# Optimization experiments

Hardware: AMD Instinct MI355X
Metric: run time of the kernel (lower is better)

## Reference

```python
import jax, jax.numpy as jnp
import numpy as np

# ---- fixed architecture constants (from init_kwargs) ----
N_WALL, N_ROOF, N_WINDOW = 4, 1, 2
N_RC = N_WALL + N_ROOF
HID = 32
ENC_LEN = 48
DT = 900.0
R_OPAQUE, C_OPAQUE = 10.0, 1.0e5
R_TRANS = 2.0
DIRECT_COEF, ABS_WALL_COEF, ABS_ROOF_COEF = 0.5, 0.5, 0.5
C_ZONE = 1.0e5
B, T = 2048, 1440


def setup_inputs() -> dict:
    key = jax.random.key(0)
    k0, k1, k2 = jax.random.split(key, 3)
    input_X = jax.random.normal(k0, (B, T, 7), dtype=jnp.float32)
    # EnvelopeRC deterministic inits
    rc_R_inv = jnp.concatenate([
        1.0 / (10.0 + 1.0 * jnp.arange(N_WALL, dtype=jnp.float32)),
        1.0 / (20.0 + 2.0 * jnp.arange(N_ROOF, dtype=jnp.float32))])
    rc_C_inv = jnp.concatenate([
        1.0 / (80.0 + 10.0 * jnp.arange(N_WALL, dtype=jnp.float32)),
        1.0 / (60.0 + 10.0 * jnp.arange(N_ROOF, dtype=jnp.float32))])
    window_R_inv = 1.0 / (1.0 + 0.1 * jnp.arange(N_WINDOW, dtype=jnp.float32))
    # Internal MLP: xavier_uniform with gain 0.1, zero bias
    lim1 = 0.1 * np.sqrt(6.0 / (2 + HID))
    int_W1 = jax.random.uniform(k1, (HID, 2), jnp.float32, -lim1, lim1)
    int_b1 = jnp.zeros((HID,), jnp.float32)
    lim2 = 0.1 * np.sqrt(6.0 / (HID + 1))
    int_W2 = jax.random.uniform(k2, (1, HID), jnp.float32, -lim2, lim2)
    int_b2 = jnp.zeros((1,), jnp.float32)
    return {
        'input_X': input_X,
        'rc_R_inv': rc_R_inv, 'rc_C_inv': rc_C_inv, 'window_R_inv': window_R_inv,
        'hvac_gain': jnp.float32(0.1),
        'int_W1': int_W1, 'int_b1': int_b1, 'int_W2': int_W2, 'int_b2': int_b2,
        'int_gain': jnp.float32(0.1),
        'direct_gain': jnp.float32(0.1), 'abs_wall': jnp.float32(0.1), 'abs_roof': jnp.float32(0.1),
        'zone_C_inv': jnp.float32(1.0 / 10000.0),
    }


def _forward(input_X, rc_R_inv, rc_C_inv, window_R_inv, hvac_gain,
             int_W1, int_b1, int_W2, int_b2, int_gain,
             direct_gain, abs_wall, abs_roof, zone_C_inv):
    sp = jax.nn.softplus
    Bn, Tn = input_X.shape[0], input_X.shape[1]
    tz_gt  = input_X[:, :, 0]   # [B,T]
    t_amb  = input_X[:, :, 1]
    sol    = input_X[:, :, 2]
    int_x  = input_X[:, :, 3:6]
    hvac_x = input_X[:, :, 6]

    # Internal MLP (state-free -> vectorized over time)
    h1  = jax.nn.relu(jnp.einsum('bti,hi->bth', int_x[:, :, :2], int_W1) + int_b1)
    sch = jax.nn.sigmoid(jnp.einsum('bth,oh->bto', h1, int_W2) + int_b2)[:, :, 0] + int_x[:, :, 2]
    q_int  = sp(int_gain) * 0.1 * sch          # [B,T]
    q_hvac = sp(hvac_gain) * 0.1 * hvac_x      # [B,T]

    # Bounded RC parameters
    r_inv   = sp(rc_R_inv) * (1.0 / R_OPAQUE)  # [n_rc]
    c_inv   = sp(rc_C_inv) * (1.0 / C_OPAQUE)  # [n_rc]
    win_rsum = jnp.sum(sp(window_R_inv)) * (1.0 / R_TRANS)
    abs_rc  = jnp.where(jnp.arange(N_RC) < N_WALL,
                        sp(abs_wall) * ABS_WALL_COEF,
                        sp(abs_roof) * ABS_ROOF_COEF)   # [n_rc]
    q_dir   = sp(direct_gain) * DIRECT_COEF * sol       # [B,T]
    cz_inv  = sp(zone_C_inv) * (1.0 / C_ZONE)

    # Initial state: Tmid_i = 0.7*Tzone0 + 0.3*Tamb0
    Tz0   = tz_gt[:, 0]                                      # [B]
    Tmid0 = jnp.broadcast_to((0.7 * Tz0 + 0.3 * t_amb[:, 0])[:, None], (Bn, N_RC))

    # Teacher forcing during encoder window: carry GT zone temp while t+1 < enc_len
    tz_gt_next = jnp.concatenate([tz_gt[:, 1:], tz_gt[:, -1:]], axis=1)  # [B,T]
    use_gt = (jnp.arange(Tn) + 1) < ENC_LEN                              # [T]

    xs = (t_amb.T, sol.T, q_dir.T, q_int.T, q_hvac.T, tz_gt_next.T, use_gt)

    def step(carry, x):
        Tz, Tmid = carry                      # [B], [B,n_rc]
        ta, so, qd, qi, qh, gt_next, ug = x
        q_in  = (ta[:, None] - Tmid) * r_inv
        q_out = (Tmid - Tz[:, None]) * r_inv
        dTmid = (q_in - q_out + so[:, None] * abs_rc) * c_inv
        q_env = jnp.sum(q_out, axis=1) + (ta - Tz) * win_rsum
        dTz   = (q_env + qi + qh + qd) * cz_inv
        Tz_new   = Tz + dTz * DT
        Tmid_new = Tmid + dTmid * DT
        Tz_carry = jnp.where(ug, gt_next, Tz_new)
        return (Tz_carry, Tmid_new), Tz_new

    _, tz_seq = jax.lax.scan(step, (Tz0, Tmid0), xs)   # [T,B]
    return jnp.transpose(tz_seq)[:, :, None]           # [B,T,1]


def reference(input_X, rc_R_inv, rc_C_inv, window_R_inv, hvac_gain,
              int_W1, int_b1, int_W2, int_b2, int_gain,
              direct_gain, abs_wall, abs_roof, zone_C_inv):
    return _forward(input_X, rc_R_inv, rc_C_inv, window_R_inv, hvac_gain,
                    int_W1, int_b1, int_W2, int_b2, int_gain,
                    direct_gain, abs_wall, abs_roof, zone_C_inv)
```

## Files before the change

kernel.cpp:

```cpp
#include <hip/hip_runtime.h>
#include <math.h>

#define BATCH 2048
#define TLEN  1440
#define T7    (TLEN * 7)
#define CL0   48
#define CL2   16
#define NCH   88
#define TREST (TLEN - CL0)

#define PACK2_OFF 0
#define PACKU_OFF (PACK2_OFF + 2 * TLEN * BATCH)
#define PACKG_OFF (PACKU_OFF + TLEN * BATCH)
#define INIT_OFF  (PACKG_OFF + 48 * BATCH)
#define E_OFF     (INIT_OFF + 2 * BATCH)
#define XC_OFF    (E_OFF + NCH * BATCH * 8)
#define A16_OFF   (XC_OFF + NCH * BATCH * 8)
#define V_OFF     (A16_OFF + 64)
#define WP_OFF    (V_OFF + 128)
#define PRM_OFF   (WP_OFF + 128)
#define WS_FLOATS (PRM_OFF + 32)

__device__ __forceinline__ float sp_precise(float x) { return log1pf(expf(x)); }

struct Prm {
  float P[5], M[5], Q[5], K[5];
  float AZ, dtczw, dtcz, cInt, cHv, cDir;
};
__device__ __forceinline__ Prm make_prm(const float* rcR, const float* rcC,
                                        const float* winR, const float* hvg,
                                        const float* ing, const float* dg,
                                        const float* aw, const float* ar,
                                        const float* zc) {
  Prm p;
  float r[5], cc[5], rsum = 0.f;
  #pragma unroll
  for (int j = 0; j < 5; ++j) {
    r[j] = sp_precise(rcR[j]) * 0.1f;
    cc[j] = sp_precise(rcC[j]) * 1e-5f;
    rsum += r[j];
  }
  float w  = (sp_precise(winR[0]) + sp_precise(winR[1])) * 0.5f;
  float cz = sp_precise(zc[0]) * 1e-5f;
  float aW = sp_precise(aw[0]) * 0.5f, aR = sp_precise(ar[0]) * 0.5f;
  float dtcz = 900.f * cz;
  #pragma unroll
  for (int j = 0; j < 5; ++j) {
    p.P[j] = 900.f * r[j] * cc[j];
    p.M[j] = 1.f - 2.f * p.P[j];
    p.Q[j] = 900.f * cc[j] * ((j < 4) ? aW : aR);
    p.K[j] = dtcz * r[j];
  }
  p.AZ = 1.f - dtcz * (w + rsum);
  p.dtczw = dtcz * w;
  p.dtcz = dtcz;
  p.cInt = sp_precise(ing[0]) * 0.1f;
  p.cHv  = sp_precise(hvg[0]) * 0.1f;
  p.cDir = sp_precise(dg[0])  * 0.5f;
  return p;
}

__global__ void k0_params(const float* __restrict__ rcR, const float* __restrict__ rcC,
                          const float* __restrict__ winR, const float* __restrict__ hvg,
                          const float* __restrict__ W1, const float* __restrict__ B1,
                          const float* __restrict__ W2, const float* __restrict__ B2,
                          const float* __restrict__ ing, const float* __restrict__ dg,
                          const float* __restrict__ aw, const float* __restrict__ ar,
                          const float* __restrict__ zc, float* __restrict__ ws) {
  __shared__ float A0s[36], Ma[36], Mb[36], vrow[2][8];
  int ln = threadIdx.x;
  if (ln < 32) {
    ((float4*)(ws + WP_OFF))[ln] =
        make_float4(W1[2 * ln], W1[2 * ln + 1], B1[ln], W2[ln]);
  }
  if (ln == 0) {
    Prm p = make_prm(rcR, rcC, winR, hvg, ing, dg, aw, ar, zc);
    float* prm = ws + PRM_OFF;
    for (int j = 0; j < 5; ++j) {
      prm[j] = p.P[j]; prm[5 + j] = p.M[j]; prm[10 + j] = p.Q[j]; prm[15 + j] = p.K[j];
    }
    prm[20] = p.AZ; prm[21] = p.dtczw; prm[22] = p.dtcz;
    prm[23] = p.cInt; prm[24] = p.cHv; prm[25] = p.cDir;
    prm[26] = B2[0];
    for (int i = 0; i < 36; ++i) A0s[i] = 0.f;
    A0s[0] = p.AZ;
    for (int j = 0; j < 5; ++j) {
      A0s[0 * 6 + 1 + j]       = p.K[j];
      A0s[(1 + j) * 6 + 0]     = p.P[j];
      A0s[(1 + j) * 6 + 1 + j] = p.M[j];
    }
  }
  __syncthreads();
  int i6 = ln / 6, j6 = ln % 6;
  bool act = ln < 36;
#define MM(DST, L, R) { if (act) { float s = 0.f; \
  for (int m = 0; m < 6; ++m) s = fmaf((L)[i6 * 6 + m], (R)[m * 6 + j6], s); \
  (DST)[ln] = s; } __syncthreads(); }
  MM(Mb, A0s, A0s);
  MM(Ma, Mb, Mb);
  MM(Mb, Ma, Ma);
  MM(Ma, Mb, Mb);
  if (act) ws[A16_OFF + ln] = Ma[ln];
  if (ln < 6) vrow[0][ln] = A0s[ln];
  __syncthreads();
  int cur = 0;
  for (int kk = 0; kk < CL2; ++kk) {
    if (ln < 6) {
      ws[V_OFF + kk * 8 + ln] = vrow[cur][ln];
      float s = 0.f;
      for (int m = 0; m < 6; ++m) s = fmaf(vrow[cur][m], A0s[m * 6 + ln], s);
      vrow[1 - cur][ln] = s;
    }
    __syncthreads();
    cur ^= 1;
  }
}

__global__ __launch_bounds__(256) void k1_pack(const float* __restrict__ X,
                                               float* __restrict__ ws) {
  __shared__ float lds[256 * 29];
  __shared__ float ldsW[128];
  int tg  = blockIdx.x >> 3;
  int b0  = (blockIdx.x & 7) << 8;
  int t0r = tg * 4;
  int tid = threadIdx.x;
  int b   = b0 + tid;
  const float* prm = ws + PRM_OFF;
  float dtczw = prm[21], dtcz = prm[22];
  float cInt = prm[23], cHv = prm[24], cDir = prm[25];
  float b2 = prm[26];
  if (tid < 32) *(float4*)&ldsW[tid * 4] = ((const float4*)(ws + WP_OFF))[tid];
  const float* base = X + ((size_t)b0 * TLEN + t0r) * 7;
  #pragma unroll
  for (int i = 0; i < 7; ++i) {
    int F = i * 256 + tid;
    int row = F / 7, q = F - row * 7;
    float4 v = *(const float4*)(base + (size_t)row * T7 + q * 4);
    int la = row * 29 + q * 4;
    lds[la] = v.x; lds[la + 1] = v.y; lds[la + 2] = v.z; lds[la + 3] = v.w;
  }
  float gtb = 0.f;
  if (t0r < 44) gtb = X[(size_t)b * T7 + (size_t)(t0r + 4) * 7];
  __syncthreads();
  int j29 = tid * 29;
  float ta[4], so[4], x3[4], x4[4], x5[4], hv[4];
  #pragma unroll
  for (int s = 0; s < 4; ++s) {
    const float* x = &lds[j29 + s * 7];
    ta[s] = x[1]; so[s] = x[2]; x3[s] = x[3]; x4[s] = x[4]; x5[s] = x[5]; hv[s] = x[6];
  }
  float acc[4] = {b2, b2, b2, b2};
  #pragma unroll
  for (int h = 0; h < 32; ++h) {
    float4 wv = *(const float4*)&ldsW[h * 4];
    #pragma unroll
    for (int s = 0; s < 4; ++s) {
      float z = fmaf(wv.x, x3[s], fmaf(wv.y, x4[s], wv.z));
      acc[s] = fmaf(wv.w, fmaxf(z, 0.f), acc[s]);
    }
  }
  float2* pk2 = (float2*)(ws + PACK2_OFF);
  float*  pu  = ws + PACKU_OFF;
  float*  pg  = ws + PACKG_OFF;
  #pragma unroll
  for (int s = 0; s < 4; ++s) {
    float sch = __frcp_rn(1.f + __expf(-acc[s])) + x5[s];
    float q = fmaf(cInt, sch, fmaf(cHv, hv[s], cDir * so[s]));
    float u = fmaf(dtczw, ta[s], dtcz * q);
    int t = t0r + s;
    size_t o = (size_t)t * BATCH + b;
    pk2[o] = make_float2(ta[s], so[s]);
    pu[o]  = u;
    if (t < 48) {
      float gt = (t < 47) ? ((s < 3) ? lds[j29 + (s + 1) * 7] : gtb) : 0.f;
      pg[o] = gt;
    }
  }
  if (tg == 0) {
    float tz0 = lds[j29], ta0 = lds[j29 + 1];
    ((float2*)(ws + INIT_OFF))[b] = make_float2(tz0, fmaf(0.7f, tz0, 0.3f * ta0));
  }
}

__global__ __launch_bounds__(256) void k2_scan(float* __restrict__ out,
                                               float* __restrict__ ws) {
  int c = blockIdx.x >> 3;
  int b = ((blockIdx.x & 7) << 8) + threadIdx.x;
  const float* prm = ws + PRM_OFF;
  float Pa[5], Mm[5], Qa[5], Ka[5];
  #pragma unroll
  for (int j = 0; j < 5; ++j) {
    Pa[j] = prm[j]; Mm[j] = prm[5 + j]; Qa[j] = prm[10 + j]; Ka[j] = prm[15 + j];
  }
  float AZ = prm[20];
  bool isc0 = (c == 0);
  int t0 = isc0 ? 0 : CL0 + (c - 1) * CL2;
  int steps = isc0 ? CL0 : CL2;
  float Tz = 0.f, T0 = 0.f, T1 = 0.f, T2 = 0.f, T3 = 0.f, T4 = 0.f;
  if (isc0) {
    float2 iv = ((const float2*)(ws + INIT_OFF))[b];
    Tz = iv.x;
    T0 = T1 = T2 = T3 = T4 = iv.y;
  }
  const float2* pk2 = ((const float2*)(ws + PACK2_OFF)) + (size_t)t0 * BATCH + b;
  const float*  pu  = ws + PACKU_OFF + (size_t)t0 * BATCH + b;
  const float*  pg  = ws + PACKG_OFF + b;
  float* op = out + (size_t)b * TLEN + t0;
  float o0 = 0.f, o1 = 0.f, o2 = 0.f;
  #pragma unroll 4
  for (int k = 0; k < steps; ++k) {
    float2 f2 = pk2[(size_t)k * BATCH];
    float  uv = pu[(size_t)k * BATCH];
    float d = fmaf(Ka[0], T0, uv);
    d = fmaf(Ka[1], T1, d); d = fmaf(Ka[2], T2, d);
    d = fmaf(Ka[3], T3, d); d = fmaf(Ka[4], T4, d);
    float tzn = fmaf(AZ, Tz, d);
    T0 = fmaf(Mm[0], T0, fmaf(Pa[0], Tz, fmaf(Pa[0], f2.x, Qa[0] * f2.y)));
    T1 = fmaf(Mm[1], T1, fmaf(Pa[1], Tz, fmaf(Pa[1], f2.x, Qa[1] * f2.y)));
    T2 = fmaf(Mm[2], T2, fmaf(Pa[2], Tz, fmaf(Pa[2], f2.x, Qa[2] * f2.y)));
    T3 = fmaf(Mm[3], T3, fmaf(Pa[3], Tz, fmaf(Pa[3], f2.x, Qa[3] * f2.y)));
    T4 = fmaf(Mm[4], T4, fmaf(Pa[4], Tz, fmaf(Pa[4], f2.x, Qa[4] * f2.y)));
    int ph = k & 3;
    if (ph == 0) o0 = tzn; else if (ph == 1) o1 = tzn;
    else if (ph == 2) o2 = tzn;
    else *(float4*)(op + (k - 3)) = make_float4(o0, o1, o2, tzn);
    if (isc0 && k < 47) Tz = pg[(size_t)k * BATCH];
    else Tz = tzn;
  }
  float* e = ws + E_OFF + ((size_t)c * BATCH + b) * 8;
  *(float4*)e       = make_float4(Tz, T0, T1, T2);
  *(float4*)(e + 4) = make_float4(T3, T4, 0.f, 0.f);
}

__global__ __launch_bounds__(64) void k2b_combine(float* __restrict__ ws) {
  int b = blockIdx.x * 64 + threadIdx.x;
  float A16r[36];
  #pragma unroll
  for (int i = 0; i < 36; ++i) A16r[i] = ws[A16_OFF + i];
  const float* e = ws + E_OFF;
  float4 h0 = *(const float4*)(e + (size_t)b * 8);
  float2 h1 = *(const float2*)(e + (size_t)b * 8 + 4);
  float Xs[6] = {h0.x, h0.y, h0.z, h0.w, h1.x, h1.y};
  for (int base = 1; base <= 87; base += 8) {
    float4 q0[8]; float2 q1[8];
    #pragma unroll
    for (int i = 0; i < 8; ++i) {
      int cI = base + i;
      if (cI <= 86) {
        const float* en = e + ((size_t)cI * BATCH + b) * 8;
        q0[i] = *(const float4*)en;
        q1[i] = *(const float2*)(en + 4);
      }
    }
    #pragma unroll
    for (int i = 0; i < 8; ++i) {
      int cI = base + i;
      if (cI > 87) break;
      float* xc = ws + XC_OFF + ((size_t)cI * BATCH + b) * 8;
      *(float4*)xc       = make_float4(Xs[0], Xs[1], Xs[2], Xs[3]);
      *(float2*)(xc + 4) = make_float2(Xs[4], Xs[5]);
      if (cI <= 86) {
        float ecur[6] = {q0[i].x, q0[i].y, q0[i].z, q0[i].w, q1[i].x, q1[i].y};
        float Y[6];
        #pragma unroll
        for (int r = 0; r < 6; ++r) {
          float s = ecur[r];
          #pragma unroll
          for (int m = 0; m < 6; ++m) s = fmaf(A16r[r * 6 + m], Xs[m], s);
          Y[r] = s;
        }
        #pragma unroll
        for (int j = 0; j < 6; ++j) Xs[j] = Y[j];
      }
    }
  }
}

__global__ __launch_bounds__(256) void k2c_correct(float* __restrict__ out,
                                                   const float* __restrict__ ws) {
  int tid = blockIdx.x * 256 + threadIdx.x;
  int b  = tid / TREST;
  int tt = tid - b * TREST;
  int c  = (tt >> 4) + 1;
  int kk = tt & 15;
  const float* xc = ws + XC_OFF + ((size_t)c * BATCH + b) * 8;
  float4 x0 = *(const float4*)xc;
  float2 x1 = *(const float2*)(xc + 4);
  const float* v = ws + V_OFF + kk * 8;
  float4 v0 = *(const float4*)v;
  float2 v1 = *(const float2*)(v + 4);
  size_t o = (size_t)b * TLEN + CL0 + tt;
  float s = out[o];
  s = fmaf(v0.x, x0.x, s); s = fmaf(v0.y, x0.y, s); s = fmaf(v0.z, x0.z, s);
  s = fmaf(v0.w, x0.w, s); s = fmaf(v1.x, x1.x, s); s = fmaf(v1.y, x1.y, s);
  out[o] = s;
}

__global__ void k_fallback(const float* __restrict__ X,
    const float* __restrict__ rcR, const float* __restrict__ rcC,
    const float* __restrict__ winR, const float* __restrict__ hvg,
    const float* __restrict__ W1, const float* __restrict__ B1,
    const float* __restrict__ W2, const float* __restrict__ B2,
    const float* __restrict__ ing, const float* __restrict__ dg,
    const float* __restrict__ aw, const float* __restrict__ ar,
    const float* __restrict__ zc, float* __restrict__ out) {
  int b = blockIdx.x * 64 + threadIdx.x;
  if (b >= BATCH) return;
  Prm p = make_prm(rcR, rcC, winR, hvg, ing, dg, aw, ar, zc);
  const float* xb = X + (size_t)b * T7;
  float Tz = xb[0];
  float tm = fmaf(0.7f, xb[0], 0.3f * xb[1]);
  float Tm[5] = {tm, tm, tm, tm, tm};
  for (int t = 0; t < TLEN; ++t) {
    const float* x = xb + t * 7;
    float ta = x[1], so = x[2], x3 = x[3], x4 = x[4], x5 = x[5], hv = x[6];
    float acc = B2[0];
    #pragma unroll
    for (int h = 0; h < 32; ++h) {
      float z = fmaf(W1[2 * h], x3, fmaf(W1[2 * h + 1], x4, B1[h]));
      acc = fmaf(W2[h], fmaxf(z, 0.f), acc);
    }
    float sch = __frcp_rn(1.f + __expf(-acc)) + x5;
    float q = fmaf(p.cInt, sch, fmaf(p.cHv, hv, p.cDir * so));
    float u = fmaf(p.dtczw, ta, p.dtcz * q);
    float d = u;
    #pragma unroll
    for (int j = 0; j < 5; ++j) d = fmaf(p.K[j], Tm[j], d);
    float tzn = fmaf(p.AZ, Tz, d);
    #pragma unroll
    for (int j = 0; j < 5; ++j)
      Tm[j] = fmaf(p.M[j], Tm[j], fmaf(p.P[j], Tz, fmaf(p.P[j], ta, p.Q[j] * so)));
    out[(size_t)b * TLEN + t] = tzn;
    Tz = (t < 47) ? x[7] : tzn;
  }
}

extern "C" void kernel_launch(void* const* d_in, const int* in_sizes, int n_in,
                              void* d_out, int out_size, void* d_ws, size_t ws_size,
                              hipStream_t stream) {
  const float* X    = (const float*)d_in[0];
  const float* rcR  = (const float*)d_in[1];
  const float* rcC  = (const float*)d_in[2];
  const float* winR = (const float*)d_in[3];
  const float* hvg  = (const float*)d_in[4];
  const float* W1   = (const float*)d_in[5];
  const float* B1   = (const float*)d_in[6];
  const float* W2   = (const float*)d_in[7];
  const float* B2   = (const float*)d_in[8];
  const float* ing  = (const float*)d_in[9];
  const float* dg   = (const float*)d_in[10];
  const float* aw   = (const float*)d_in[11];
  const float* ar   = (const float*)d_in[12];
  const float* zc   = (const float*)d_in[13];
  float* out = (float*)d_out;
  float* ws  = (float*)d_ws;

  if (ws_size >= (size_t)WS_FLOATS * sizeof(float)) {
    k0_params<<<1, 64, 0, stream>>>(rcR, rcC, winR, hvg, W1, B1, W2, B2,
                                    ing, dg, aw, ar, zc, ws);
    k1_pack<<<(TLEN / 4) * 8, 256, 0, stream>>>(X, ws);
    k2_scan<<<NCH * 8, 256, 0, stream>>>(out, ws);
    k2b_combine<<<32, 64, 0, stream>>>(ws);
    k2c_correct<<<(BATCH * TREST) / 256, 256, 0, stream>>>(out, ws);
  } else {
    k_fallback<<<BATCH / 64, 64, 0, stream>>>(X, rcR, rcC, winR, hvg, W1, B1, W2, B2,
                                              ing, dg, aw, ar, zc, out);
  }
}
```

Measured before the change: 214.9 us.

## Remove params kernel; recompute parameters per kernel and prefetch scan inputs

Drops the single-block parameter kernel and recomputes the softplus-derived coefficients inside each remaining kernel. The combine kernel now builds A^16 in registers, and the correction kernel computes its row vector by iterating up to 15 steps per thread. The scan kernel is split into a first-chunk branch and a generic branch, and each preloads 16 timesteps of packed inputs into registers before the recurrence. This removes one launch and a serial dependency but adds redundant transcendental and matrix math per thread, which is notable in the elementwise correction kernel.

```diff
diff --git a/kernel.cpp b/kernel.cpp
--- a/kernel.cpp
+++ b/kernel.cpp
@@ -15,11 +15,7 @@
 #define INIT_OFF  (PACKG_OFF + 48 * BATCH)
 #define E_OFF     (INIT_OFF + 2 * BATCH)
 #define XC_OFF    (E_OFF + NCH * BATCH * 8)
-#define A16_OFF   (XC_OFF + NCH * BATCH * 8)
-#define V_OFF     (A16_OFF + 64)
-#define WP_OFF    (V_OFF + 128)
-#define PRM_OFF   (WP_OFF + 128)
-#define WS_FLOATS (PRM_OFF + 32)
+#define WS_FLOATS (XC_OFF + NCH * BATCH * 8)
 
 __device__ __forceinline__ float sp_precise(float x) { return log1pf(expf(x)); }
 
@@ -60,64 +56,14 @@
   return p;
 }
 
-__global__ void k0_params(const float* __restrict__ rcR, const float* __restrict__ rcC,
-                          const float* __restrict__ winR, const float* __restrict__ hvg,
-                          const float* __restrict__ W1, const float* __restrict__ B1,
-                          const float* __restrict__ W2, const float* __restrict__ B2,
-                          const float* __restrict__ ing, const float* __restrict__ dg,
-                          const float* __restrict__ aw, const float* __restrict__ ar,
-                          const float* __restrict__ zc, float* __restrict__ ws) {
-  __shared__ float A0s[36], Ma[36], Mb[36], vrow[2][8];
-  int ln = threadIdx.x;
-  if (ln < 32) {
-    ((float4*)(ws + WP_OFF))[ln] =
-        make_float4(W1[2 * ln], W1[2 * ln + 1], B1[ln], W2[ln]);
-  }
-  if (ln == 0) {
-    Prm p = make_prm(rcR, rcC, winR, hvg, ing, dg, aw, ar, zc);
-    float* prm = ws + PRM_OFF;
-    for (int j = 0; j < 5; ++j) {
-      prm[j] = p.P[j]; prm[5 + j] = p.M[j]; prm[10 + j] = p.Q[j]; prm[15 + j] = p.K[j];
-    }
-    prm[20] = p.AZ; prm[21] = p.dtczw; prm[22] = p.dtcz;
-    prm[23] = p.cInt; prm[24] = p.cHv; prm[25] = p.cDir;
-    prm[26] = B2[0];
-    for (int i = 0; i < 36; ++i) A0s[i] = 0.f;
-    A0s[0] = p.AZ;
-    for (int j = 0; j < 5; ++j) {
-      A0s[0 * 6 + 1 + j]       = p.K[j];
-      A0s[(1 + j) * 6 + 0]     = p.P[j];
-      A0s[(1 + j) * 6 + 1 + j] = p.M[j];
-    }
-  }
-  __syncthreads();
-  int i6 = ln / 6, j6 = ln % 6;
-  bool act = ln < 36;
-#define MM(DST, L, R) { if (act) { float s = 0.f; \
-  for (int m = 0; m < 6; ++m) s = fmaf((L)[i6 * 6 + m], (R)[m * 6 + j6], s); \
-  (DST)[ln] = s; } __syncthreads(); }
-  MM(Mb, A0s, A0s);
-  MM(Ma, Mb, Mb);
-  MM(Mb, Ma, Ma);
-  MM(Ma, Mb, Mb);
-  if (act) ws[A16_OFF + ln] = Ma[ln];
-  if (ln < 6) vrow[0][ln] = A0s[ln];
-  __syncthreads();
-  int cur = 0;
-  for (int kk = 0; kk < CL2; ++kk) {
-    if (ln < 6) {
-      ws[V_OFF + kk * 8 + ln] = vrow[cur][ln];
-      float s = 0.f;
-      for (int m = 0; m < 6; ++m) s = fmaf(vrow[cur][m], A0s[m * 6 + ln], s);
-      vrow[1 - cur][ln] = s;
-    }
-    __syncthreads();
-    cur ^= 1;
-  }
-}
-
 __global__ __launch_bounds__(256) void k1_pack(const float* __restrict__ X,
-                                               float* __restrict__ ws) {
+    const float* __restrict__ rcR, const float* __restrict__ rcC,
+    const float* __restrict__ winR, const float* __restrict__ hvg,
+    const float* __restrict__ W1, const float* __restrict__ B1,
+    const float* __restrict__ W2, const float* __restrict__ B2,
+    const float* __restrict__ ing, const float* __restrict__ dg,
+    const float* __restrict__ aw, const float* __restrict__ ar,
+    const float* __restrict__ zc, float* __restrict__ ws) {
   __shared__ float lds[256 * 29];
   __shared__ float ldsW[128];
   int tg  = blockIdx.x >> 3;
@@ -125,11 +71,14 @@
   int t0r = tg * 4;
   int tid = threadIdx.x;
   int b   = b0 + tid;
-  const float* prm = ws + PRM_OFF;
-  float dtczw = prm[21], dtcz = prm[22];
-  float cInt = prm[23], cHv = prm[24], cDir = prm[25];
-  float b2 = prm[26];
-  if (tid < 32) *(float4*)&ldsW[tid * 4] = ((const float4*)(ws + WP_OFF))[tid];
+  Prm p = make_prm(rcR, rcC, winR, hvg, ing, dg, aw, ar, zc);
+  float b2 = B2[0];
+  if (tid < 32) {
+    ldsW[tid * 4 + 0] = W1[2 * tid];
+    ldsW[tid * 4 + 1] = W1[2 * tid + 1];
+    ldsW[tid * 4 + 2] = B1[tid];
+    ldsW[tid * 4 + 3] = W2[tid];
+  }
   const float* base = X + ((size_t)b0 * TLEN + t0r) * 7;
   #pragma unroll
   for (int i = 0; i < 7; ++i) {
@@ -165,8 +114,8 @@
   #pragma unroll
   for (int s = 0; s < 4; ++s) {
     float sch = __frcp_rn(1.f + __expf(-acc[s])) + x5[s];
-    float q = fmaf(cInt, sch, fmaf(cHv, hv[s], cDir * so[s]));
-    float u = fmaf(dtczw, ta[s], dtcz * q);
+    float q = fmaf(p.cInt, sch, fmaf(p.cHv, hv[s], p.cDir * so[s]));
+    float u = fmaf(p.dtczw, ta[s], p.dtcz * q);
     int t = t0r + s;
     size_t o = (size_t)t * BATCH + b;
     pk2[o] = make_float2(ta[s], so[s]);
@@ -182,61 +131,119 @@
   }
 }
 
-__global__ __launch_bounds__(256) void k2_scan(float* __restrict__ out,
-                                               float* __restrict__ ws) {
+__global__ __launch_bounds__(256) void k2_scan(
+    const float* __restrict__ rcR, const float* __restrict__ rcC,
+    const float* __restrict__ winR, const float* __restrict__ hvg,
+    const float* __restrict__ ing, const float* __restrict__ dg,
+    const float* __restrict__ aw, const float* __restrict__ ar,
+    const float* __restrict__ zc,
+    float* __restrict__ out, float* __restrict__ ws) {
   int c = blockIdx.x >> 3;
   int b = ((blockIdx.x & 7) << 8) + threadIdx.x;
-  const float* prm = ws + PRM_OFF;
-  float Pa[5], Mm[5], Qa[5], Ka[5];
-  #pragma unroll
-  for (int j = 0; j < 5; ++j) {
-    Pa[j] = prm[j]; Mm[j] = prm[5 + j]; Qa[j] = prm[10 + j]; Ka[j] = prm[15 + j];
-  }
-  float AZ = prm[20];
-  bool isc0 = (c == 0);
-  int t0 = isc0 ? 0 : CL0 + (c - 1) * CL2;
-  int steps = isc0 ? CL0 : CL2;
-  float Tz = 0.f, T0 = 0.f, T1 = 0.f, T2 = 0.f, T3 = 0.f, T4 = 0.f;
-  if (isc0) {
+  Prm p = make_prm(rcR, rcC, winR, hvg, ing, dg, aw, ar, zc);
+  float Tz, T0, T1, T2, T3, T4;
+  if (c == 0) {
     float2 iv = ((const float2*)(ws + INIT_OFF))[b];
-    Tz = iv.x;
-    T0 = T1 = T2 = T3 = T4 = iv.y;
-  }
-  const float2* pk2 = ((const float2*)(ws + PACK2_OFF)) + (size_t)t0 * BATCH + b;
-  const float*  pu  = ws + PACKU_OFF + (size_t)t0 * BATCH + b;
-  const float*  pg  = ws + PACKG_OFF + b;
-  float* op = out + (size_t)b * TLEN + t0;
-  float o0 = 0.f, o1 = 0.f, o2 = 0.f;
-  #pragma unroll 4
-  for (int k = 0; k < steps; ++k) {
-    float2 f2 = pk2[(size_t)k * BATCH];
-    float  uv = pu[(size_t)k * BATCH];
-    float d = fmaf(Ka[0], T0, uv);
-    d = fmaf(Ka[1], T1, d); d = fmaf(Ka[2], T2, d);
-    d = fmaf(Ka[3], T3, d); d = fmaf(Ka[4], T4, d);
-    float tzn = fmaf(AZ, Tz, d);
-    T0 = fmaf(Mm[0], T0, fmaf(Pa[0], Tz, fmaf(Pa[0], f2.x, Qa[0] * f2.y)));
-    T1 = fmaf(Mm[1], T1, fmaf(Pa[1], Tz, fmaf(Pa[1], f2.x, Qa[1] * f2.y)));
-    T2 = fmaf(Mm[2], T2, fmaf(Pa[2], Tz, fmaf(Pa[2], f2.x, Qa[2] * f2.y)));
-    T3 = fmaf(Mm[3], T3, fmaf(Pa[3], Tz, fmaf(Pa[3], f2.x, Qa[3] * f2.y)));
-    T4 = fmaf(Mm[4], T4, fmaf(Pa[4], Tz, fmaf(Pa[4], f2.x, Qa[4] * f2.y)));
-    int ph = k & 3;
-    if (ph == 0) o0 = tzn; else if (ph == 1) o1 = tzn;
-    else if (ph == 2) o2 = tzn;
-    else *(float4*)(op + (k - 3)) = make_float4(o0, o1, o2, tzn);
-    if (isc0 && k < 47) Tz = pg[(size_t)k * BATCH];
-    else Tz = tzn;
+    Tz = iv.x; T0 = T1 = T2 = T3 = T4 = iv.y;
+    const float2* pk2 = ((const float2*)(ws + PACK2_OFF)) + b;
+    const float*  pu  = ws + PACKU_OFF + b;
+    const float*  pg  = ws + PACKG_OFF + b;
+    float* op = out + (size_t)b * TLEN;
+    for (int g = 0; g < 3; ++g) {
+      float2 f2[16]; float uv[16], gt[16];
+      #pragma unroll
+      for (int k = 0; k < 16; ++k) {
+        size_t o = (size_t)(g * 16 + k) * BATCH;
+        f2[k] = pk2[o]; uv[k] = pu[o]; gt[k] = pg[o];
+      }
+      float o0 = 0.f, o1 = 0.f, o2 = 0.f;
+      #pragma unroll
+      for (int k = 0; k < 16; ++k) {
+        float d = fmaf(p.K[0], T0, uv[k]);
+        d = fmaf(p.K[1], T1, d); d = fmaf(p.K[2], T2, d);
+        d = fmaf(p.K[3], T3, d); d = fmaf(p.K[4], T4, d);
+        float tzn = fmaf(p.AZ, Tz, d);
+        #pragma unroll
+        for (int j = 0; j < 5; ++j) {
+          float* T = (j == 0) ? &T0 : (j == 1) ? &T1 : (j == 2) ? &T2 : (j == 3) ? &T3 : &T4;
+          *T = fmaf(p.M[j], *T, fmaf(p.P[j], Tz, fmaf(p.P[j], f2[k].x, p.Q[j] * f2[k].y)));
+        }
+        int ph = k & 3;
+        if (ph == 0) o0 = tzn; else if (ph == 1) o1 = tzn;
+        else if (ph == 2) o2 = tzn;
+        else *(float4*)(op + g * 16 + (k - 3)) = make_float4(o0, o1, o2, tzn);
+        Tz = (g * 16 + k < 47) ? gt[k] : tzn;
+      }
+    }
+  } else {
+    int t0 = CL0 + (c - 1) * CL2;
+    const float2* pk2 = ((const float2*)(ws + PACK2_OFF)) + (size_t)t0 * BATCH + b;
+    const float*  pu  = ws + PACKU_OFF + (size_t)t0 * BATCH + b;
+    float2 f2[16]; float uv[16];
+    #pragma unroll
+    for (int k = 0; k < 16; ++k) {
+      f2[k] = pk2[(size_t)k * BATCH];
+      uv[k] = pu[(size_t)k * BATCH];
+    }
+    Tz = 0.f; T0 = T1 = T2 = T3 = T4 = 0.f;
+    float* op = out + (size_t)b * TLEN + t0;
+    float o0 = 0.f, o1 = 0.f, o2 = 0.f;
+    #pragma unroll
+    for (int k = 0; k < 16; ++k) {
+      float d = fmaf(p.K[0], T0, uv[k]);
+      d = fmaf(p.K[1], T1, d); d = fmaf(p.K[2], T2, d);
+      d = fmaf(p.K[3], T3, d); d = fmaf(p.K[4], T4, d);
+      float tzn = fmaf(p.AZ, Tz, d);
+      T0 = fmaf(p.M[0], T0, fmaf(p.P[0], Tz, fmaf(p.P[0], f2[k].x, p.Q[0] * f2[k].y)));
+      T1 = fmaf(p.M[1], T1, fmaf(p.P[1], Tz, fmaf(p.P[1], f2[k].x, p.Q[1] * f2[k].y)));
+      T2 = fmaf(p.M[2], T2, fmaf(p.P[2], Tz, fmaf(p.P[2], f2[k].x, p.Q[2] * f2[k].y)));
+      T3 = fmaf(p.M[3], T3, fmaf(p.P[3], Tz, fmaf(p.P[3], f2[k].x, p.Q[3] * f2[k].y)));
+      T4 = fmaf(p.M[4], T4, fmaf(p.P[4], Tz, fmaf(p.P[4], f2[k].x, p.Q[4] * f2[k].y)));
+      int ph = k & 3;
+      if (ph == 0) o0 = tzn; else if (ph == 1) o1 = tzn;
+      else if (ph == 2) o2 = tzn;
+      else *(float4*)(op + (k - 3)) = make_float4(o0, o1, o2, tzn);
+      Tz = tzn;
+    }
   }
   float* e = ws + E_OFF + ((size_t)c * BATCH + b) * 8;
   *(float4*)e       = make_float4(Tz, T0, T1, T2);
   *(float4*)(e + 4) = make_float4(T3, T4, 0.f, 0.f);
 }
 
-__global__ __launch_bounds__(64) void k2b_combine(float* __restrict__ ws) {
+__global__ __launch_bounds__(64) void k2b_combine(
+    const float* __restrict__ rcR, const float* __restrict__ rcC,
+    const float* __restrict__ winR, const float* __restrict__ hvg,
+    const float* __restrict__ ing, const float* __restrict__ dg,
+    const float* __restrict__ aw, const float* __restrict__ ar,
+    const float* __restrict__ zc, float* __restrict__ ws) {
   int b = blockIdx.x * 64 + threadIdx.x;
-  float A16r[36];
-  #pragma unroll
-  for (int i = 0; i < 36; ++i) A16r[i] = ws[A16_OFF + i];
+  Prm p = make_prm(rcR, rcC, winR, hvg, ing, dg, aw, ar, zc);
+  float A[36];
+  #pragma unroll
+  for (int i = 0; i < 36; ++i) A[i] = 0.f;
+  A[0] = p.AZ;
+  #pragma unroll
+  for (int j = 0; j < 5; ++j) {
+    A[1 + j]             = p.K[j];
+    A[(1 + j) * 6]       = p.P[j];
+    A[(1 + j) * 6 + 1 + j] = p.M[j];
+  }
+  #pragma unroll
+  for (int it = 0; it < 4; ++it) {
+    float Bm[36];
+    #pragma unroll
+    for (int i = 0; i < 6; ++i)
+      #pragma unroll
+      for (int j = 0; j < 6; ++j) {
+        float s = 0.f;
+        #pragma unroll
+        for (int m = 0; m < 6; ++m) s = fmaf(A[i * 6 + m], A[m * 6 + j], s);
+        Bm[i * 6 + j] = s;
+      }
+    #pragma unroll
+    for (int i = 0; i < 36; ++i) A[i] = Bm[i];
+  }
   const float* e = ws + E_OFF;
   float4 h0 = *(const float4*)(e + (size_t)b * 8);
   float2 h1 = *(const float2*)(e + (size_t)b * 8 + 4);
@@ -266,7 +273,7 @@
         for (int r = 0; r < 6; ++r) {
           float s = ecur[r];
           #pragma unroll
-          for (int m = 0; m < 6; ++m) s = fmaf(A16r[r * 6 + m], Xs[m], s);
+          for (int m = 0; m < 6; ++m) s = fmaf(A[r * 6 + m], Xs[m], s);
           Y[r] = s;
         }
         #pragma unroll
@@ -276,23 +283,38 @@
   }
 }
 
-__global__ __launch_bounds__(256) void k2c_correct(float* __restrict__ out,
-                                                   const float* __restrict__ ws) {
+__global__ __launch_bounds__(256) void k2c_correct(
+    const float* __restrict__ rcR, const float* __restrict__ rcC,
+    const float* __restrict__ winR, const float* __restrict__ hvg,
+    const float* __restrict__ ing, const float* __restrict__ dg,
+    const float* __restrict__ aw, const float* __restrict__ ar,
+    const float* __restrict__ zc,
+    float* __restrict__ out, const float* __restrict__ ws) {
   int tid = blockIdx.x * 256 + threadIdx.x;
   int b  = tid / TREST;
   int tt = tid - b * TREST;
   int c  = (tt >> 4) + 1;
   int kk = tt & 15;
+  Prm p = make_prm(rcR, rcC, winR, hvg, ing, dg, aw, ar, zc);
+  float v0 = p.AZ, v1 = p.K[0], v2 = p.K[1], v3 = p.K[2], v4 = p.K[3], v5 = p.K[4];
+  for (int i = 0; i < kk; ++i) {
+    float n0 = v0 * p.AZ;
+    n0 = fmaf(v1, p.P[0], n0); n0 = fmaf(v2, p.P[1], n0); n0 = fmaf(v3, p.P[2], n0);
+    n0 = fmaf(v4, p.P[3], n0); n0 = fmaf(v5, p.P[4], n0);
+    float n1 = fmaf(v0, p.K[0], v1 * p.M[0]);
+    float n2 = fmaf(v0, p.K[1], v2 * p.M[1]);
+    float n3 = fmaf(v0, p.K[2], v3 * p.M[2]);
+    float n4 = fmaf(v0, p.K[3], v4 * p.M[3]);
+    float n5 = fmaf(v0, p.K[4], v5 * p.M[4]);
+    v0 = n0; v1 = n1; v2 = n2; v3 = n3; v4 = n4; v5 = n5;
+  }
   const float* xc = ws + XC_OFF + ((size_t)c * BATCH + b) * 8;
   float4 x0 = *(const float4*)xc;
   float2 x1 = *(const float2*)(xc + 4);
-  const float* v = ws + V_OFF + kk * 8;
-  float4 v0 = *(const float4*)v;
-  float2 v1 = *(const float2*)(v + 4);
   size_t o = (size_t)b * TLEN + CL0 + tt;
   float s = out[o];
-  s = fmaf(v0.x, x0.x, s); s = fmaf(v0.y, x0.y, s); s = fmaf(v0.z, x0.z, s);
-  s = fmaf(v0.w, x0.w, s); s = fmaf(v1.x, x1.x, s); s = fmaf(v1.y, x1.y, s);
+  s = fmaf(v0, x0.x, s); s = fmaf(v1, x0.y, s); s = fmaf(v2, x0.z, s);
+  s = fmaf(v3, x0.w, s); s = fmaf(v4, x1.x, s); s = fmaf(v5, x1.y, s);
   out[o] = s;
 }
 
@@ -356,12 +378,13 @@
   float* ws  = (float*)d_ws;
 
   if (ws_size >= (size_t)WS_FLOATS * sizeof(float)) {
-    k0_params<<<1, 64, 0, stream>>>(rcR, rcC, winR, hvg, W1, B1, W2, B2,
-                                    ing, dg, aw, ar, zc, ws);
-    k1_pack<<<(TLEN / 4) * 8, 256, 0, stream>>>(X, ws);
-    k2_scan<<<NCH * 8, 256, 0, stream>>>(out, ws);
-    k2b_combine<<<32, 64, 0, stream>>>(ws);
-    k2c_correct<<<(BATCH * TREST) / 256, 256, 0, stream>>>(out, ws);
+    k1_pack<<<(TLEN / 4) * 8, 256, 0, stream>>>(X, rcR, rcC, winR, hvg,
+                                                W1, B1, W2, B2, ing, dg, aw, ar, zc, ws);
+    k2_scan<<<NCH * 8, 256, 0, stream>>>(rcR, rcC, winR, hvg, ing, dg, aw, ar, zc,
+                                         out, ws);
+    k2b_combine<<<32, 64, 0, stream>>>(rcR, rcC, winR, hvg, ing, dg, aw, ar, zc, ws);
+    k2c_correct<<<(BATCH * TREST) / 256, 256, 0, stream>>>(rcR, rcC, winR, hvg,
+                                                           ing, dg, aw, ar, zc, out, ws);
   } else {
     k_fallback<<<BATCH / 64, 64, 0, stream>>>(X, rcR, rcC, winR, hvg, W1, B1, W2, B2,
                                               ing, dg, aw, ar, zc, out);
```

New measurement: 303.5 us. +41.2%, slower.
